# Performance work log

Measured on AMD Instinct MI355X. Metric: run time of the kernel, lower is better.

## Reference

```python
import jax, jax.numpy as jnp
import numpy as np

D = 768          # n_embd
I = 3072         # moe_intermediate_size (4 * n_embd)
E = 8            # n_routed_experts
K = 2            # num_experts_per_tok
LIMIT = 10.0     # swiglu_limit
VOCAB = 32768


def setup_inputs() -> dict:
    key = jax.random.key(0)
    ks = jax.random.split(key, 10)
    s = 0.02
    return {
        "x": jax.random.normal(ks[0], (1, 2048, D), dtype=jnp.float32),
        "input_ids": jax.random.randint(ks[1], (1, 2048), 0, VOCAB, dtype=jnp.int64),
        "gate_w": jax.random.normal(ks[2], (D, E), dtype=jnp.float32) * s,
        "gate_bias": jnp.zeros((E,), dtype=jnp.float32),
        "w1": jax.random.normal(ks[3], (E, D, I), dtype=jnp.float32) * s,
        "w2": jax.random.normal(ks[4], (E, I, D), dtype=jnp.float32) * s,
        "w3": jax.random.normal(ks[5], (E, D, I), dtype=jnp.float32) * s,
        "w1s": jax.random.normal(ks[6], (D, I), dtype=jnp.float32) * s,
        "w2s": jax.random.normal(ks[7], (I, D), dtype=jnp.float32) * s,
        "w3s": jax.random.normal(ks[8], (D, I), dtype=jnp.float32) * s,
    }


def _expert(xf, W1, W2, W3):
    # SwiGLU with asymmetric clamping, as in DeepSeekExpert (swiglu_limit > 0)
    gate = jnp.minimum(xf @ W1, LIMIT)               # clamp max only
    up = jnp.clip(xf @ W3, -LIMIT, LIMIT)            # clamp both sides
    return (jax.nn.silu(gate) * up) @ W2


def reference(x, input_ids, gate_w, gate_bias, w1, w2, w3, w1s, w2s, w3s):
    B, T, _ = x.shape
    flat = x.reshape(-1, D)                           # [N, D], N = B*T
    N = flat.shape[0]

    # gating: sqrtsoftplus scoring
    scores = jnp.sqrt(jax.nn.softplus(flat @ gate_w))  # [N, E]
    routed_scores = scores + gate_bias                 # gate_bias used only for topk selection
    _, indices = jax.lax.top_k(routed_scores, K)       # [N, K]

    weights = jnp.take_along_axis(scores, indices, axis=1)  # [N, K]
    # norm_topk_prob=True; routed_scaling_factor=1.0
    weights = weights / jnp.clip(weights.sum(axis=-1, keepdims=True), 1e-6)

    # dense combine matrix [N, E] (jit-friendly dispatch/combine)
    combine = jnp.zeros((N, E), dtype=weights.dtype)
    combine = combine.at[jnp.arange(N)[:, None], indices].add(weights)

    # shared expert on all tokens
    y = _expert(flat, w1s, w2s, w3s)                   # [N, D]

    # routed experts: batched grouped GEMM over all tokens, then weighted combine
    gate_h = jnp.minimum(jnp.einsum('td,edi->eti', flat, w1), LIMIT)   # [E, N, I]
    up_h = jnp.clip(jnp.einsum('td,edi->eti', flat, w3), -LIMIT, LIMIT)
    h = jax.nn.silu(gate_h) * up_h                     # [E, N, I]
    out_e = jnp.einsum('eti,eid->etd', h, w2)          # [E, N, D]
    routed = jnp.einsum('etd,te->td', out_e, combine)  # [N, D]

    return (y + routed).reshape(B, T, D)
```

## Files before the change

### kernel.cpp

```cpp
#include <hip/hip_runtime.h>


#define D_ 768
#define I_ 3072
#define E_ 8
#define NTOK 2048
#define NPMAX 5120
#define MAXTILES 40
#define NSHT 16
#define ROWS (NTOK + NPMAX)
#define SPLITK 2
#define KS_ (I_ / SPLITK)

typedef __bf16 bf16x8 __attribute__((ext_vector_type(8)));
typedef float floatx4 __attribute__((ext_vector_type(4)));

#define GLOAD_LDS16(g, l) __builtin_amdgcn_global_load_lds( \
    (const __attribute__((address_space(1))) void*)(g),     \
    (__attribute__((address_space(3))) void*)(l), 16, 0, 0)

__device__ __forceinline__ unsigned short f2b(float f) {
    unsigned int u = __float_as_uint(f);
    u += 0x7fffu + ((u >> 16) & 1u);
    return (unsigned short)(u >> 16);
}


__global__ __launch_bounds__(256) void prep_kernel(
    const float* __restrict__ x, const float* __restrict__ gw,
    const float* __restrict__ gbias,
    const float* __restrict__ w1, const float* __restrict__ w2,
    const float* __restrict__ w3, const float* __restrict__ w1s,
    const float* __restrict__ w2s, const float* __restrict__ w3s,
    unsigned short* __restrict__ xb,
    unsigned short* __restrict__ w1b, unsigned short* __restrict__ w3b,
    unsigned short* __restrict__ w2b, unsigned short* __restrict__ w1sb,
    unsigned short* __restrict__ w3sb, unsigned short* __restrict__ w2sb,
    int* __restrict__ idx, float* __restrict__ wts) {
    __shared__ float t[64][65];
    int b = blockIdx.x, tid = threadIdx.x;
    if (b < 15552) {
        const float* s; unsigned short* d; int R, C, bx, by;
        if (b < 10368) {
            int z = b / 576, r = b % 576; bx = r % 48; by = r / 48; R = D_; C = I_;
            if (z < 8)       { s = w1 + (size_t)z * D_ * I_;       d = w1b + (size_t)z * D_ * I_; }
            else if (z < 16) { s = w3 + (size_t)(z - 8) * D_ * I_; d = w3b + (size_t)(z - 8) * D_ * I_; }
            else if (z == 16){ s = w1s; d = w1sb; }
            else             { s = w3s; d = w3sb; }
        } else {
            int bb = b - 10368;
            int z = bb / 576, r = bb % 576; bx = r % 12; by = r / 12; R = I_; C = D_;
            if (z < 8) { s = w2 + (size_t)z * I_ * D_; d = w2b + (size_t)z * I_ * D_; }
            else       { s = w2s; d = w2sb; }
        }
        int c0 = bx * 64, r0 = by * 64;
#pragma unroll
        for (int j = 0; j < 4; j++) {
            int slot = tid + j * 256;
            int rr = slot >> 4, c4 = (slot & 15) * 4;
            float4 v = *(const float4*)(s + (size_t)(r0 + rr) * C + c0 + c4);
            t[rr][c4] = v.x; t[rr][c4 + 1] = v.y; t[rr][c4 + 2] = v.z; t[rr][c4 + 3] = v.w;
        }
        __syncthreads();
#pragma unroll
        for (int j = 0; j < 2; j++) {
            int slot = tid + j * 256;
            int c = slot >> 3, rs = (slot & 7) * 8;
            unsigned short o[8] __attribute__((aligned(16)));
#pragma unroll
            for (int i = 0; i < 8; i++) o[i] = f2b(t[rs + i][c]);
            *(int4*)(d + (size_t)(c0 + c) * R + r0 + rs) = *(const int4*)o;
        }
    } else if (b < 17088) {
        int gid = (b - 15552) * 256 + tid;
        float4 v = *(const float4*)(x + (size_t)gid * 4);
        ushort4 o;
        o.x = f2b(v.x); o.y = f2b(v.y); o.z = f2b(v.z); o.w = f2b(v.w);
        *(ushort4*)(xb + (size_t)gid * 4) = o;
    } else {
        int tok = (b - 17088) * 4 + (tid >> 6);
        int lane = tid & 63;
        float z[E_];
#pragma unroll
        for (int e = 0; e < E_; e++) z[e] = 0.f;
        const float* xr = x + (size_t)tok * D_;
        for (int j = lane; j < D_; j += 64) {
            float xv = xr[j];
            const float* g = gw + (size_t)j * E_;
#pragma unroll
            for (int e = 0; e < E_; e++) z[e] += xv * g[e];
        }
#pragma unroll
        for (int off = 32; off > 0; off >>= 1)
#pragma unroll
            for (int e = 0; e < E_; e++) z[e] += __shfl_down(z[e], off, 64);
        if (lane == 0) {
            float s[E_], r[E_];
#pragma unroll
            for (int e = 0; e < E_; e++) {
                float zz = z[e];
                float sp = zz > 0.f ? zz + log1pf(expf(-zz)) : log1pf(expf(zz));
                s[e] = sqrtf(sp);
                r[e] = s[e] + gbias[e];
            }
            int i0 = 0;
            for (int e = 1; e < E_; e++) if (r[e] > r[i0]) i0 = e;
            int i1 = (i0 == 0) ? 1 : 0;
            for (int e = 0; e < E_; e++) if (e != i0 && r[e] > r[i1]) i1 = e;
            float w0 = s[i0], w1v = s[i1];
            float inv = 1.f / fmaxf(w0 + w1v, 1e-6f);
            idx[2 * tok] = i0; idx[2 * tok + 1] = i1;
            wts[2 * tok] = w0 * inv; wts[2 * tok + 1] = w1v * inv;
        }
    }
}


__global__ void route_build_kernel(const int* __restrict__ idx,
                                   const float* __restrict__ wts,
                                   int* __restrict__ pair_token,
                                   float* __restrict__ pair_w,
                                   int* __restrict__ pos_of,
                                   int* __restrict__ tiles) {
    __shared__ int cnt[E_], seg[E_], cur[E_];
    int tid = threadIdx.x;
    if (tid < E_) { cnt[tid] = 0; cur[tid] = 0; }
    __syncthreads();
    for (int p = tid; p < NTOK * 2; p += 256) atomicAdd(&cnt[idx[p]], 1);
    __syncthreads();
    if (tid == 0) {
        int off = 0, nt = 0;
        for (int e = 0; e < E_; e++) {
            seg[e] = off;
            int te = (cnt[e] + 127) >> 7;
            for (int j = 0; j < te; j++) {
                tiles[nt * 2] = e; tiles[nt * 2 + 1] = off + j * 128; nt++;
            }
            off += te * 128;
        }
        for (; nt < MAXTILES; nt++) { tiles[nt * 2] = -1; tiles[nt * 2 + 1] = 0; }
    }
    for (int p = tid; p < NPMAX; p += 256) pair_token[p] = -1;
    __syncthreads();
    for (int p = tid; p < NTOK * 2; p += 256) {
        int e = idx[p];
        int r = atomicAdd(&cur[e], 1);
        int pos = seg[e] + r;
        pair_token[pos] = p >> 1;
        pair_w[pos] = wts[p];
        pos_of[p] = pos;
    }
}


__launch_bounds__(256)
__global__ void gemm_act_kernel(const unsigned short* __restrict__ xb,
                                const unsigned short* __restrict__ w1sb,
                                const unsigned short* __restrict__ w3sb,
                                const unsigned short* __restrict__ w1b,
                                const unsigned short* __restrict__ w3b,
                                const int* __restrict__ tiles,
                                const int* __restrict__ pair_token,
                                unsigned short* __restrict__ act) {
    __shared__ __align__(16) unsigned short As[128 * 64];
    __shared__ __align__(16) unsigned short Bs1[64 * 64];
    __shared__ __align__(16) unsigned short Bs3[64 * 64];

    int mt = blockIdx.y;
    const unsigned short *B1, *B3;
    int m0; bool routed;
    if (mt < NSHT) {
        B1 = w1sb; B3 = w3sb; m0 = mt * 128; routed = false;
    } else {
        int e = tiles[(mt - NSHT) * 2];
        if (e < 0) return;
        m0 = NTOK + tiles[(mt - NSHT) * 2 + 1];
        B1 = w1b + (size_t)e * I_ * D_; B3 = w3b + (size_t)e * I_ * D_;
        routed = true;
    }
    int n0 = blockIdx.x * 64;
    int tid = threadIdx.x;
    int lane = tid & 63, wave = tid >> 6;
    int wm = (wave & 1) * 64, wn = (wave >> 1) * 32;
    int l15 = lane & 15, quad = lane >> 4;

    int rl = lane >> 3;
    int ph = lane & 7;
    int lg = ph ^ rl;
    const unsigned short* asrc[4];
#pragma unroll
    for (int j = 0; j < 4; j++) {
        int r = j * 32 + wave * 8 + rl;
        int tok;
        if (routed) { tok = pair_token[m0 - NTOK + r]; if (tok < 0) tok = 0; }
        else tok = m0 + r;
        asrc[j] = xb + (size_t)tok * D_ + lg * 8;
    }
    const unsigned short *b1src[2], *b3src[2];
#pragma unroll
    for (int j = 0; j < 2; j++) {
        int r = j * 32 + wave * 8 + rl;
        b1src[j] = B1 + (size_t)(n0 + r) * D_ + lg * 8;
        b3src[j] = B3 + (size_t)(n0 + r) * D_ + lg * 8;
    }
    unsigned short *ldA[4], *ldB1[2], *ldB3[2];
#pragma unroll
    for (int j = 0; j < 4; j++) ldA[j] = As + (j * 32 + wave * 8) * 64;
#pragma unroll
    for (int j = 0; j < 2; j++) {
        ldB1[j] = Bs1 + (j * 32 + wave * 8) * 64;
        ldB3[j] = Bs3 + (j * 32 + wave * 8) * 64;
    }

    floatx4 acc1[4][2] = {}; floatx4 acc3[4][2] = {};
    int sx = (l15 & 7);

    for (int k0 = 0; k0 < D_; k0 += 64) {
        __syncthreads();
#pragma unroll
        for (int j = 0; j < 4; j++) GLOAD_LDS16(asrc[j] + k0, ldA[j]);
#pragma unroll
        for (int j = 0; j < 2; j++) {
            GLOAD_LDS16(b1src[j] + k0, ldB1[j]);
            GLOAD_LDS16(b3src[j] + k0, ldB3[j]);
        }
        __syncthreads();

#pragma unroll
        for (int kk = 0; kk < 2; kk++) {
            int pq = ((kk * 4 + quad) ^ sx) * 8;
            bf16x8 af[4], b1f[2], b3f[2];
#pragma unroll
            for (int mi = 0; mi < 4; mi++)
                af[mi] = *(const bf16x8*)(As + (wm + mi * 16 + l15) * 64 + pq);
#pragma unroll
            for (int ni = 0; ni < 2; ni++) {
                b1f[ni] = *(const bf16x8*)(Bs1 + (wn + ni * 16 + l15) * 64 + pq);
                b3f[ni] = *(const bf16x8*)(Bs3 + (wn + ni * 16 + l15) * 64 + pq);
            }
#pragma unroll
            for (int mi = 0; mi < 4; mi++)
#pragma unroll
                for (int ni = 0; ni < 2; ni++) {
                    acc1[mi][ni] = __builtin_amdgcn_mfma_f32_16x16x32_bf16(
                        af[mi], b1f[ni], acc1[mi][ni], 0, 0, 0);
                    acc3[mi][ni] = __builtin_amdgcn_mfma_f32_16x16x32_bf16(
                        af[mi], b3f[ni], acc3[mi][ni], 0, 0, 0);
                }
        }
    }

#pragma unroll
    for (int mi = 0; mi < 4; mi++)
#pragma unroll
        for (int ni = 0; ni < 2; ni++) {
            int col = n0 + wn + ni * 16 + l15;
#pragma unroll
            for (int rr = 0; rr < 4; rr++) {
                int row = m0 + wm + mi * 16 + quad * 4 + rr;
                float g = fminf(acc1[mi][ni][rr], 10.f);
                float u = fminf(fmaxf(acc3[mi][ni][rr], -10.f), 10.f);
                float a = g / (1.f + __expf(-g)) * u;
                act[(size_t)row * I_ + col] = f2b(a);
            }
        }
}


__launch_bounds__(256)
__global__ void gemm_out_kernel(const unsigned short* __restrict__ act,
                                const unsigned short* __restrict__ w2sb,
                                const unsigned short* __restrict__ w2b,
                                const int* __restrict__ tiles,
                                float* __restrict__ outp) {
    __shared__ __align__(16) unsigned short As[128 * 64];
    __shared__ __align__(16) unsigned short Bs[64 * 64];

    int mt = blockIdx.y, ks = blockIdx.z;
    int kbase = ks * KS_;
    const unsigned short* B;
    int m0;
    if (mt < NSHT) {
        B = w2sb; m0 = mt * 128;
    } else {
        int e = tiles[(mt - NSHT) * 2];
        if (e < 0) return;
        m0 = NTOK + tiles[(mt - NSHT) * 2 + 1];
        B = w2b + (size_t)e * I_ * D_;
    }
    float* C = outp + (size_t)ks * ROWS * D_;
    int n0 = blockIdx.x * 64;
    int tid = threadIdx.x;
    int lane = tid & 63, wave = tid >> 6;
    int wm = (wave & 1) * 64, wn = (wave >> 1) * 32;
    int l15 = lane & 15, quad = lane >> 4;

    int rl = lane >> 3, ph = lane & 7, lg = ph ^ rl;
    const unsigned short* asrc[4];
#pragma unroll
    for (int j = 0; j < 4; j++)
        asrc[j] = act + (size_t)(m0 + j * 32 + wave * 8 + rl) * I_ + kbase + lg * 8;
    const unsigned short* bsrc[2];
#pragma unroll
    for (int j = 0; j < 2; j++)
        bsrc[j] = B + (size_t)(n0 + j * 32 + wave * 8 + rl) * I_ + kbase + lg * 8;
    unsigned short *ldA[4], *ldB[2];
#pragma unroll
    for (int j = 0; j < 4; j++) ldA[j] = As + (j * 32 + wave * 8) * 64;
#pragma unroll
    for (int j = 0; j < 2; j++) ldB[j] = Bs + (j * 32 + wave * 8) * 64;

    floatx4 acc[4][2] = {};
    int sx = (l15 & 7);

    for (int k0 = 0; k0 < KS_; k0 += 64) {
        __syncthreads();
#pragma unroll
        for (int j = 0; j < 4; j++) GLOAD_LDS16(asrc[j] + k0, ldA[j]);
#pragma unroll
        for (int j = 0; j < 2; j++) GLOAD_LDS16(bsrc[j] + k0, ldB[j]);
        __syncthreads();

#pragma unroll
        for (int kk = 0; kk < 2; kk++) {
            int pq = ((kk * 4 + quad) ^ sx) * 8;
            bf16x8 af[4], bf[2];
#pragma unroll
            for (int mi = 0; mi < 4; mi++)
                af[mi] = *(const bf16x8*)(As + (wm + mi * 16 + l15) * 64 + pq);
#pragma unroll
            for (int ni = 0; ni < 2; ni++)
                bf[ni] = *(const bf16x8*)(Bs + (wn + ni * 16 + l15) * 64 + pq);
#pragma unroll
            for (int mi = 0; mi < 4; mi++)
#pragma unroll
                for (int ni = 0; ni < 2; ni++)
                    acc[mi][ni] = __builtin_amdgcn_mfma_f32_16x16x32_bf16(
                        af[mi], bf[ni], acc[mi][ni], 0, 0, 0);
        }
    }

#pragma unroll
    for (int mi = 0; mi < 4; mi++)
#pragma unroll
        for (int ni = 0; ni < 2; ni++) {
            int col = n0 + wn + ni * 16 + l15;
#pragma unroll
            for (int rr = 0; rr < 4; rr++) {
                int row = m0 + wm + mi * 16 + quad * 4 + rr;
                C[(size_t)row * D_ + col] = acc[mi][ni][rr];
            }
        }
}


__global__ void combine_kernel(const float* __restrict__ outp,
                               const int* __restrict__ pos_of,
                               const float* __restrict__ pair_w,
                               float* __restrict__ out) {
    int gid = blockIdx.x * 256 + threadIdx.x;
    int t = gid / (D_ / 4);
    int j = (gid % (D_ / 4)) * 4;
    int p0 = pos_of[2 * t], p1 = pos_of[2 * t + 1];
    float w0 = pair_w[p0], w1 = pair_w[p1];
    float a0 = 0.f, a1 = 0.f, a2 = 0.f, a3 = 0.f;
#pragma unroll
    for (int ks = 0; ks < SPLITK; ks++) {
        const float* P = outp + (size_t)ks * ROWS * D_;
        float4 a = *(const float4*)(P + (size_t)t * D_ + j);
        float4 b = *(const float4*)(P + (size_t)(NTOK + p0) * D_ + j);
        float4 c = *(const float4*)(P + (size_t)(NTOK + p1) * D_ + j);
        a0 += a.x + w0 * b.x + w1 * c.x;
        a1 += a.y + w0 * b.y + w1 * c.y;
        a2 += a.z + w0 * b.z + w1 * c.z;
        a3 += a.w + w0 * b.w + w1 * c.w;
    }
    float4 o; o.x = a0; o.y = a1; o.z = a2; o.w = a3;
    *(float4*)(out + (size_t)t * D_ + j) = o;
}


extern "C" void kernel_launch(void* const* d_in, const int* in_sizes, int n_in,
                              void* d_out, int out_size, void* d_ws, size_t ws_size,
                              hipStream_t stream) {
    (void)in_sizes; (void)n_in; (void)out_size; (void)ws_size;
    const float* x   = (const float*)d_in[0];
    const float* gw  = (const float*)d_in[2];
    const float* gb  = (const float*)d_in[3];
    const float* w1  = (const float*)d_in[4];
    const float* w2  = (const float*)d_in[5];
    const float* w3  = (const float*)d_in[6];
    const float* w1s = (const float*)d_in[7];
    const float* w2s = (const float*)d_in[8];
    const float* w3s = (const float*)d_in[9];
    float* out = (float*)d_out;

    char* ws = (char*)d_ws;
    size_t off = 0;
    auto alloc = [&](size_t bytes) {
        size_t o = (off + 255) & ~(size_t)255;
        off = o + bytes;
        return (void*)(ws + o);
    };
    unsigned short* xb   = (unsigned short*)alloc((size_t)NTOK * D_ * 2);
    unsigned short* w1b  = (unsigned short*)alloc((size_t)E_ * I_ * D_ * 2);
    unsigned short* w3b  = (unsigned short*)alloc((size_t)E_ * I_ * D_ * 2);
    unsigned short* w2b  = (unsigned short*)alloc((size_t)E_ * I_ * D_ * 2);
    unsigned short* w1sb = (unsigned short*)alloc((size_t)I_ * D_ * 2);
    unsigned short* w3sb = (unsigned short*)alloc((size_t)I_ * D_ * 2);
    unsigned short* w2sb = (unsigned short*)alloc((size_t)I_ * D_ * 2);
    unsigned short* act  = (unsigned short*)alloc((size_t)ROWS * I_ * 2);
    float* outp = (float*)alloc((size_t)SPLITK * ROWS * D_ * 4);
    int*   idx  = (int*)alloc((size_t)NTOK * 2 * 4);
    float* wts  = (float*)alloc((size_t)NTOK * 2 * 4);
    int*   ptok = (int*)alloc((size_t)NPMAX * 4);
    float* pw   = (float*)alloc((size_t)NPMAX * 4);
    int*   posf = (int*)alloc((size_t)NTOK * 2 * 4);
    int*   tls  = (int*)alloc((size_t)MAXTILES * 2 * 4);

    prep_kernel<<<17600, 256, 0, stream>>>(x, gw, gb, w1, w2, w3, w1s, w2s, w3s,
                                           xb, w1b, w3b, w2b, w1sb, w3sb, w2sb,
                                           idx, wts);
    route_build_kernel<<<1, 256, 0, stream>>>(idx, wts, ptok, pw, posf, tls);
    gemm_act_kernel<<<dim3(I_ / 64, NSHT + MAXTILES), 256, 0, stream>>>(
        xb, w1sb, w3sb, w1b, w3b, tls, ptok, act);
    gemm_out_kernel<<<dim3(D_ / 64, NSHT + MAXTILES, SPLITK), 256, 0, stream>>>(
        act, w2sb, w2b, tls, outp);
    combine_kernel<<<NTOK * (D_ / 4) / 256, 256, 0, stream>>>(outp, posf, pw, out);
}
```

Measured before the change: 465.7 us.

## Overlap w2 weight conversion with first GEMM by interleaving blocks

Moves the fp32-to-bf16 transpose of w2/w2s out of the prep kernel and into the gemm_act kernel as extra blocks interleaved along grid y (two conversion rows per GEMM row). The intent is to hide the memory-bound conversion of w2 behind the compute-bound gate/up GEMM and to shorten the serial prep kernel. The trade-off is a larger grid, shared LDS reuse and possible contention between the conversion traffic and GEMM loads. Routed GEMM tiles that exit early still occupy grid slots.

```diff
diff --git a/kernel.cpp b/kernel.cpp
--- a/kernel.cpp
+++ b/kernel.cpp
@@ -12,6 +12,8 @@
 #define SPLITK 2
 #define KS_ (I_ / SPLITK)
 
+#define NT2 5184
+
 typedef __bf16 bf16x8 __attribute__((ext_vector_type(8)));
 typedef float floatx4 __attribute__((ext_vector_type(4)));
 
@@ -29,30 +31,23 @@
 __global__ __launch_bounds__(256) void prep_kernel(
     const float* __restrict__ x, const float* __restrict__ gw,
     const float* __restrict__ gbias,
-    const float* __restrict__ w1, const float* __restrict__ w2,
-    const float* __restrict__ w3, const float* __restrict__ w1s,
-    const float* __restrict__ w2s, const float* __restrict__ w3s,
+    const float* __restrict__ w1, const float* __restrict__ w3,
+    const float* __restrict__ w1s, const float* __restrict__ w3s,
     unsigned short* __restrict__ xb,
     unsigned short* __restrict__ w1b, unsigned short* __restrict__ w3b,
-    unsigned short* __restrict__ w2b, unsigned short* __restrict__ w1sb,
-    unsigned short* __restrict__ w3sb, unsigned short* __restrict__ w2sb,
+    unsigned short* __restrict__ w1sb, unsigned short* __restrict__ w3sb,
     int* __restrict__ idx, float* __restrict__ wts) {
     __shared__ float t[64][65];
     int b = blockIdx.x, tid = threadIdx.x;
-    if (b < 15552) {
-        const float* s; unsigned short* d; int R, C, bx, by;
-        if (b < 10368) {
-            int z = b / 576, r = b % 576; bx = r % 48; by = r / 48; R = D_; C = I_;
-            if (z < 8)       { s = w1 + (size_t)z * D_ * I_;       d = w1b + (size_t)z * D_ * I_; }
-            else if (z < 16) { s = w3 + (size_t)(z - 8) * D_ * I_; d = w3b + (size_t)(z - 8) * D_ * I_; }
-            else if (z == 16){ s = w1s; d = w1sb; }
-            else             { s = w3s; d = w3sb; }
-        } else {
-            int bb = b - 10368;
-            int z = bb / 576, r = bb % 576; bx = r % 12; by = r / 12; R = I_; C = D_;
-            if (z < 8) { s = w2 + (size_t)z * I_ * D_; d = w2b + (size_t)z * I_ * D_; }
-            else       { s = w2s; d = w2sb; }
-        }
+    if (b < 10368) {
+        const float* s; unsigned short* d;
+        int z = b / 576, r = b % 576;
+        int bx = r % 48, by = r / 48;
+        const int R = D_, C = I_;
+        if (z < 8)       { s = w1 + (size_t)z * D_ * I_;       d = w1b + (size_t)z * D_ * I_; }
+        else if (z < 16) { s = w3 + (size_t)(z - 8) * D_ * I_; d = w3b + (size_t)(z - 8) * D_ * I_; }
+        else if (z == 16){ s = w1s; d = w1sb; }
+        else             { s = w3s; d = w3sb; }
         int c0 = bx * 64, r0 = by * 64;
 #pragma unroll
         for (int j = 0; j < 4; j++) {
@@ -71,14 +66,14 @@
             for (int i = 0; i < 8; i++) o[i] = f2b(t[rs + i][c]);
             *(int4*)(d + (size_t)(c0 + c) * R + r0 + rs) = *(const int4*)o;
         }
-    } else if (b < 17088) {
-        int gid = (b - 15552) * 256 + tid;
+    } else if (b < 11904) {
+        int gid = (b - 10368) * 256 + tid;
         float4 v = *(const float4*)(x + (size_t)gid * 4);
         ushort4 o;
         o.x = f2b(v.x); o.y = f2b(v.y); o.z = f2b(v.z); o.w = f2b(v.w);
         *(ushort4*)(xb + (size_t)gid * 4) = o;
     } else {
-        int tok = (b - 17088) * 4 + (tid >> 6);
+        int tok = (b - 11904) * 4 + (tid >> 6);
         int lane = tid & 63;
         float z[E_];
 #pragma unroll
@@ -161,12 +156,52 @@
                                 const unsigned short* __restrict__ w3b,
                                 const int* __restrict__ tiles,
                                 const int* __restrict__ pair_token,
-                                unsigned short* __restrict__ act) {
-    __shared__ __align__(16) unsigned short As[128 * 64];
-    __shared__ __align__(16) unsigned short Bs1[64 * 64];
-    __shared__ __align__(16) unsigned short Bs3[64 * 64];
-
-    int mt = blockIdx.y;
+                                unsigned short* __restrict__ act,
+                                const float* __restrict__ w2,
+                                const float* __restrict__ w2s,
+                                unsigned short* __restrict__ w2b,
+                                unsigned short* __restrict__ w2sb) {
+    __shared__ __align__(16) unsigned short smem[128 * 64 + 64 * 64 + 64 * 64];
+    unsigned short* As  = smem;
+    unsigned short* Bs1 = smem + 128 * 64;
+    unsigned short* Bs3 = smem + 128 * 64 + 64 * 64;
+
+    int bxi = blockIdx.x, byi = blockIdx.y;
+    int tid = threadIdx.x;
+
+    if (byi % 3) {
+        int slot = byi - byi / 3 - 1;
+        int b2 = slot * 48 + bxi;
+        if (b2 >= NT2) return;
+        float (*t)[65] = (float(*)[65])smem;
+        const float* s; unsigned short* dst;
+        int z = b2 / 576, r = b2 % 576;
+        int tx = r % 12, ty = r / 12;
+        const int R = I_, C = D_;
+        if (z < 8) { s = w2 + (size_t)z * I_ * D_; dst = w2b + (size_t)z * I_ * D_; }
+        else       { s = w2s; dst = w2sb; }
+        int c0 = tx * 64, r0 = ty * 64;
+#pragma unroll
+        for (int j = 0; j < 4; j++) {
+            int sl = tid + j * 256;
+            int rr = sl >> 4, c4 = (sl & 15) * 4;
+            float4 v = *(const float4*)(s + (size_t)(r0 + rr) * C + c0 + c4);
+            t[rr][c4] = v.x; t[rr][c4 + 1] = v.y; t[rr][c4 + 2] = v.z; t[rr][c4 + 3] = v.w;
+        }
+        __syncthreads();
+#pragma unroll
+        for (int j = 0; j < 2; j++) {
+            int sl = tid + j * 256;
+            int c = sl >> 3, rs = (sl & 7) * 8;
+            unsigned short o[8] __attribute__((aligned(16)));
+#pragma unroll
+            for (int i = 0; i < 8; i++) o[i] = f2b(t[rs + i][c]);
+            *(int4*)(dst + (size_t)(c0 + c) * R + r0 + rs) = *(const int4*)o;
+        }
+        return;
+    }
+
+    int mt = byi / 3;
     const unsigned short *B1, *B3;
     int m0; bool routed;
     if (mt < NSHT) {
@@ -178,8 +213,7 @@
         B1 = w1b + (size_t)e * I_ * D_; B3 = w3b + (size_t)e * I_ * D_;
         routed = true;
     }
-    int n0 = blockIdx.x * 64;
-    int tid = threadIdx.x;
+    int n0 = bxi * 64;
     int lane = tid & 63, wave = tid >> 6;
     int wm = (wave & 1) * 64, wn = (wave >> 1) * 32;
     int l15 = lane & 15, quad = lane >> 4;
@@ -418,12 +452,11 @@
     int*   posf = (int*)alloc((size_t)NTOK * 2 * 4);
     int*   tls  = (int*)alloc((size_t)MAXTILES * 2 * 4);
 
-    prep_kernel<<<17600, 256, 0, stream>>>(x, gw, gb, w1, w2, w3, w1s, w2s, w3s,
-                                           xb, w1b, w3b, w2b, w1sb, w3sb, w2sb,
-                                           idx, wts);
+    prep_kernel<<<12416, 256, 0, stream>>>(x, gw, gb, w1, w3, w1s, w3s,
+                                           xb, w1b, w3b, w1sb, w3sb, idx, wts);
     route_build_kernel<<<1, 256, 0, stream>>>(idx, wts, ptok, pw, posf, tls);
-    gemm_act_kernel<<<dim3(I_ / 64, NSHT + MAXTILES), 256, 0, stream>>>(
-        xb, w1sb, w3sb, w1b, w3b, tls, ptok, act);
+    gemm_act_kernel<<<dim3(I_ / 64, 168), 256, 0, stream>>>(
+        xb, w1sb, w3sb, w1b, w3b, tls, ptok, act, w2, w2s, w2b, w2sb);
     gemm_out_kernel<<<dim3(D_ / 64, NSHT + MAXTILES, SPLITK), 256, 0, stream>>>(
         act, w2sb, w2b, tls, outp);
     combine_kernel<<<NTOK * (D_ / 4) / 256, 256, 0, stream>>>(outp, posf, pw, out);
```

Measured after the change: 461.8 us. About the same (-0.8%).
